# Kernel optimization log

Measured on AMD Instinct MI355X. Metric: run time of the kernel, lower is better.

Reference implementation:

```python
import jax, jax.numpy as jnp
import numpy as np

N_NODES = 50000
N_EDGES = 600000
N_RELS = 500
D = 128


def setup_inputs() -> dict:
    key = jax.random.key(0)
    ks = jax.random.split(key, 8)
    h = jax.random.normal(ks[0], (N_NODES, D), dtype=jnp.float32)
    norm = jax.random.uniform(ks[1], (N_NODES, 1), dtype=jnp.float32)
    rel_emb = jax.random.normal(ks[2], (N_RELS, D), dtype=jnp.float32)
    # xavier-uniform-like scale for square weights
    lim = np.sqrt(6.0 / (D + D)) * np.sqrt(2.0)
    W_neighbor = jax.random.uniform(ks[3], (D, D), dtype=jnp.float32, minval=-lim, maxval=lim)
    loop_weight = jax.random.uniform(ks[4], (D, D), dtype=jnp.float32, minval=-lim, maxval=lim)
    edge_src = jax.random.randint(ks[5], (N_EDGES,), 0, N_NODES, dtype=jnp.int64 if jax.config.jax_enable_x64 else jnp.int32)
    edge_dst = jax.random.randint(ks[6], (N_EDGES,), 0, N_NODES, dtype=edge_src.dtype)
    edge_type = jax.random.randint(ks[7], (N_EDGES,), 0, N_RELS, dtype=edge_src.dtype)
    return {
        "h": h, "norm": norm, "rel_emb": rel_emb,
        "W_neighbor": W_neighbor, "loop_weight": loop_weight,
        "edge_src": edge_src, "edge_dst": edge_dst, "edge_type": edge_type,
    }


def reference(h, norm, rel_emb, W_neighbor, loop_weight, edge_src, edge_dst, edge_type):
    # self-loop message (dense GEMM on node features)
    loop_message = h @ loop_weight  # [N, D]

    # msg_func: gather rel emb + src features, compose ('sub' branch computes node + relation
    # in the original source, reproduced faithfully), dense matmul per edge
    relation = rel_emb[edge_type]          # [E, D] gather
    node = h[edge_src]                     # [E, D] gather
    msg = (node + relation) @ W_neighbor   # [E, D]

    # fn.sum aggregate: scatter-sum messages into destination nodes
    agg = jax.ops.segment_sum(msg, edge_dst, num_segments=h.shape[0])  # [N, D]

    # apply_func: multiply by per-node norm
    node_repr = agg * norm  # [N, D]

    # self_loop add, then activation (relu); dropout=0.0 -> identity
    node_repr = jax.nn.relu(node_repr + loop_message)
    return node_repr
```

## Files before the change

kernel.cpp:

```cpp
#include <hip/hip_runtime.h>

#define NN 50000
#define NE 600000
#define NR 500
#define DD 128
#define CAP 64

#define OFF_CUR  0
#define OFF_BKT  (NN)
#define OFF_HB   (OFF_BKT + NN * CAP)
#define OFF_RELB (OFF_HB + NN * DD / 2)
#define OFF_BP   (OFF_RELB + NR * DD / 2)
#define OFF_AGB  (OFF_BP + 16384)

typedef __bf16 bf16x8 __attribute__((ext_vector_type(8)));
typedef float  f32x4  __attribute__((ext_vector_type(4)));

#define HB_BLOCKS   3125
#define RELB_BLOCKS 32
#define PB_BLOCKS   128

__global__ __launch_bounds__(256) void prep(
    const float* __restrict__ h, const float* __restrict__ rel,
    const float* __restrict__ W, const float* __restrict__ L,
    __bf16* __restrict__ h_bf, __bf16* __restrict__ rel_bf,
    __bf16* __restrict__ Bp)
{
    int b = blockIdx.x;
    if (b < HB_BLOCKS) {
        int t = b * 256 + threadIdx.x;
        const float4* src = (const float4*)h + (size_t)t * 2;
        float4 v0 = src[0], v1 = src[1];
        bf16x8 o;
        o[0]=(__bf16)v0.x; o[1]=(__bf16)v0.y; o[2]=(__bf16)v0.z; o[3]=(__bf16)v0.w;
        o[4]=(__bf16)v1.x; o[5]=(__bf16)v1.y; o[6]=(__bf16)v1.z; o[7]=(__bf16)v1.w;
        *(bf16x8*)(h_bf + (size_t)t * 8) = o;
    } else if (b < HB_BLOCKS + RELB_BLOCKS) {
        int t = (b - HB_BLOCKS) * 256 + threadIdx.x;
        if (t < NR * DD / 8) {
            const float4* src = (const float4*)rel + (size_t)t * 2;
            float4 v0 = src[0], v1 = src[1];
            bf16x8 o;
            o[0]=(__bf16)v0.x; o[1]=(__bf16)v0.y; o[2]=(__bf16)v0.z; o[3]=(__bf16)v0.w;
            o[4]=(__bf16)v1.x; o[5]=(__bf16)v1.y; o[6]=(__bf16)v1.z; o[7]=(__bf16)v1.w;
            *(bf16x8*)(rel_bf + (size_t)t * 8) = o;
        }
    } else {
        int t = (b - HB_BLOCKS - RELB_BLOCKS) * 256 + threadIdx.x;
        int lane  = (t >> 3) & 63;
        int ntile = (t >> 9) & 7;
        int kstep = t >> 12;
        int n = ntile * 16 + (lane & 15);
        int k = kstep * 32 + (lane >> 4) * 8 + (t & 7);
        float v = (k < DD) ? W[k * DD + n] : L[(k - DD) * DD + n];
        Bp[t] = (__bf16)v;
    }
}

__global__ __launch_bounds__(256) void fill_bucket(
    const int* __restrict__ esrc, const int* __restrict__ edst,
    const int* __restrict__ etyp, int* __restrict__ cursor,
    unsigned* __restrict__ bucket)
{
    int e = blockIdx.x * 256 + threadIdx.x;
    if (e < NE) {
        int d = edst[e];
        int pos = atomicAdd(&cursor[d], 1);
        if (pos < CAP)
            bucket[(size_t)d * CAP + pos] = (unsigned)esrc[e] | ((unsigned)etyp[e] << 16);
    }
}

__global__ __launch_bounds__(256) void gather_nodes(
    const __bf16* __restrict__ h_bf, const __bf16* __restrict__ rel_bf,
    const float* __restrict__ norm, const int* __restrict__ cursor,
    const unsigned* __restrict__ bucket, __bf16* __restrict__ agg_bf)
{
    int node = (blockIdx.x * 256 + threadIdx.x) >> 4;
    int lane = threadIdx.x & 15;
    if (node >= NN) return;
    int n = cursor[node];
    n = (n < CAP) ? n : CAP;
    const unsigned* bk = bucket + (size_t)node * CAP;
    float acc[8];
#pragma unroll
    for (int j = 0; j < 8; ++j) acc[j] = 0.f;
    int i = 0;
    for (; i + 1 < n; i += 2) {
        unsigned p0 = bk[i], p1 = bk[i + 1];
        bf16x8 a0 = *(const bf16x8*)(h_bf   + (size_t)(p0 & 0xFFFFu) * DD + lane * 8);
        bf16x8 b0 = *(const bf16x8*)(rel_bf + (size_t)(p0 >> 16)     * DD + lane * 8);
        bf16x8 a1 = *(const bf16x8*)(h_bf   + (size_t)(p1 & 0xFFFFu) * DD + lane * 8);
        bf16x8 b1 = *(const bf16x8*)(rel_bf + (size_t)(p1 >> 16)     * DD + lane * 8);
#pragma unroll
        for (int j = 0; j < 8; ++j)
            acc[j] += ((float)a0[j] + (float)b0[j]) + ((float)a1[j] + (float)b1[j]);
    }
    if (i < n) {
        unsigned p0 = bk[i];
        bf16x8 a0 = *(const bf16x8*)(h_bf   + (size_t)(p0 & 0xFFFFu) * DD + lane * 8);
        bf16x8 b0 = *(const bf16x8*)(rel_bf + (size_t)(p0 >> 16)     * DD + lane * 8);
#pragma unroll
        for (int j = 0; j < 8; ++j) acc[j] += (float)a0[j] + (float)b0[j];
    }
    float sc = norm[node];
    bf16x8 o;
#pragma unroll
    for (int j = 0; j < 8; ++j) o[j] = (__bf16)(acc[j] * sc);
    *(bf16x8*)(agg_bf + (size_t)node * DD + lane * 8) = o;
}

#define AP 264

__global__ __launch_bounds__(256) void fused_mfma(
    const __bf16* __restrict__ h_bf, const __bf16* __restrict__ agg_bf,
    const __bf16* __restrict__ Bp, float* __restrict__ out)
{
    __shared__ __bf16 As[64 * AP];
    int tid = threadIdx.x;
    int row0 = blockIdx.x * 64;

#pragma unroll
    for (int it = 0; it < 8; ++it) {
        int idx = it * 256 + tid;
        int r = idx >> 5;
        int q = idx & 31;
        int gr = row0 + r;
        bf16x8 v = (bf16x8)(__bf16)0.f;
        if (gr < NN) {
            v = (q < 16)
                ? *(const bf16x8*)(agg_bf + (size_t)gr * DD + q * 8)
                : *(const bf16x8*)(h_bf   + (size_t)gr * DD + (q - 16) * 8);
        }
        *(bf16x8*)&As[r * AP + q * 8] = v;
    }
    __syncthreads();

    int lane = tid & 63;
    int wave = tid >> 6;
    int m0 = wave * 16;
    int aoff_base = (m0 + (lane & 15)) * AP + (lane >> 4) * 8;

    f32x4 acc[8];
#pragma unroll
    for (int i = 0; i < 8; ++i) acc[i] = (f32x4)0.f;

#pragma unroll
    for (int kstep = 0; kstep < 8; ++kstep) {
        bf16x8 a = *(const bf16x8*)&As[aoff_base + kstep * 32];
        const __bf16* bbase = Bp + ((size_t)(kstep * 8) * 64 + lane) * 8;
#pragma unroll
        for (int nt = 0; nt < 8; ++nt) {
            bf16x8 b = *(const bf16x8*)(bbase + (size_t)nt * 64 * 8);
            acc[nt] = __builtin_amdgcn_mfma_f32_16x16x32_bf16(a, b, acc[nt], 0, 0, 0);
        }
    }

    int quad = lane >> 4;
    int col_l = lane & 15;
#pragma unroll
    for (int nt = 0; nt < 8; ++nt) {
#pragma unroll
        for (int reg = 0; reg < 4; ++reg) {
            int gr = row0 + m0 + quad * 4 + reg;
            if (gr < NN)
                out[(size_t)gr * DD + nt * 16 + col_l] = fmaxf(acc[nt][reg], 0.f);
        }
    }
}

extern "C" void kernel_launch(void* const* d_in, const int* in_sizes, int n_in,
                              void* d_out, int out_size, void* d_ws, size_t ws_size,
                              hipStream_t stream) {
    const float* h    = (const float*)d_in[0];
    const float* norm = (const float*)d_in[1];
    const float* rel  = (const float*)d_in[2];
    const float* W    = (const float*)d_in[3];
    const float* L    = (const float*)d_in[4];
    const int* esrc   = (const int*)d_in[5];
    const int* edst   = (const int*)d_in[6];
    const int* etyp   = (const int*)d_in[7];
    float* out = (float*)d_out;

    int* ws = (int*)d_ws;
    int* cursor      = ws + OFF_CUR;
    unsigned* bucket = (unsigned*)(ws + OFF_BKT);
    __bf16* h_bf     = (__bf16*)(ws + OFF_HB);
    __bf16* rel_bf   = (__bf16*)(ws + OFF_RELB);
    __bf16* Bp       = (__bf16*)(ws + OFF_BP);
    __bf16* agg_bf   = (__bf16*)(ws + OFF_AGB);

    hipMemsetAsync(cursor, 0, (size_t)NN * sizeof(int), stream);
    prep<<<HB_BLOCKS + RELB_BLOCKS + PB_BLOCKS, 256, 0, stream>>>(
        h, rel, W, L, h_bf, rel_bf, Bp);
    fill_bucket<<<(NE + 255) / 256, 256, 0, stream>>>(esrc, edst, etyp, cursor, bucket);
    gather_nodes<<<NN * 16 / 256, 256, 0, stream>>>(h_bf, rel_bf, norm, cursor,
                                                    bucket, agg_bf);
    fused_mfma<<<(NN + 63) / 64, 256, 0, stream>>>(h_bf, agg_bf, Bp, out);
}
```

Measured before the change: 175.9 us.

## Fuse neighbor gather into MFMA GEMM kernel and fold cursor memset into prep

The per-node gather/aggregate is moved into the GEMM kernel, which writes the normalized aggregate straight into shared memory instead of round-tripping it through a global bf16 buffer. Each node now gets 4 threads with 32 accumulators each, rather than 16 threads with 8. The cursor memset is replaced by extra blocks in the prep kernel, removing a separate launch. The trade-off is less memory-level parallelism per node in the gather, higher register pressure, and only 782 blocks doing the latency-bound gather phase.

New measurement: 207.6 us. 18.0% more time.

```diff
diff --git a/kernel.cpp b/kernel.cpp
--- a/kernel.cpp
+++ b/kernel.cpp
@@ -11,7 +11,6 @@
 #define OFF_HB   (OFF_BKT + NN * CAP)
 #define OFF_RELB (OFF_HB + NN * DD / 2)
 #define OFF_BP   (OFF_RELB + NR * DD / 2)
-#define OFF_AGB  (OFF_BP + 16384)
 
 typedef __bf16 bf16x8 __attribute__((ext_vector_type(8)));
 typedef float  f32x4  __attribute__((ext_vector_type(4)));
@@ -19,12 +18,14 @@
 #define HB_BLOCKS   3125
 #define RELB_BLOCKS 32
 #define PB_BLOCKS   128
+#define CZ_BLOCKS   196
+#define PREP_BLOCKS (HB_BLOCKS + RELB_BLOCKS + PB_BLOCKS + CZ_BLOCKS)
 
 __global__ __launch_bounds__(256) void prep(
     const float* __restrict__ h, const float* __restrict__ rel,
     const float* __restrict__ W, const float* __restrict__ L,
     __bf16* __restrict__ h_bf, __bf16* __restrict__ rel_bf,
-    __bf16* __restrict__ Bp)
+    __bf16* __restrict__ Bp, int* __restrict__ cursor)
 {
     int b = blockIdx.x;
     if (b < HB_BLOCKS) {
@@ -45,7 +46,7 @@
             o[4]=(__bf16)v1.x; o[5]=(__bf16)v1.y; o[6]=(__bf16)v1.z; o[7]=(__bf16)v1.w;
             *(bf16x8*)(rel_bf + (size_t)t * 8) = o;
         }
-    } else {
+    } else if (b < HB_BLOCKS + RELB_BLOCKS + PB_BLOCKS) {
         int t = (b - HB_BLOCKS - RELB_BLOCKS) * 256 + threadIdx.x;
         int lane  = (t >> 3) & 63;
         int ntile = (t >> 9) & 7;
@@ -54,6 +55,9 @@
         int k = kstep * 32 + (lane >> 4) * 8 + (t & 7);
         float v = (k < DD) ? W[k * DD + n] : L[(k - DD) * DD + n];
         Bp[t] = (__bf16)v;
+    } else {
+        int t = (b - HB_BLOCKS - RELB_BLOCKS - PB_BLOCKS) * 256 + threadIdx.x;
+        if (t < NN) cursor[t] = 0;
     }
 }
 
@@ -71,68 +75,86 @@
     }
 }
 
-__global__ __launch_bounds__(256) void gather_nodes(
+#define AP 264
+
+__global__ __launch_bounds__(256) void fused_gather_mfma(
     const __bf16* __restrict__ h_bf, const __bf16* __restrict__ rel_bf,
     const float* __restrict__ norm, const int* __restrict__ cursor,
-    const unsigned* __restrict__ bucket, __bf16* __restrict__ agg_bf)
-{
-    int node = (blockIdx.x * 256 + threadIdx.x) >> 4;
-    int lane = threadIdx.x & 15;
-    if (node >= NN) return;
-    int n = cursor[node];
-    n = (n < CAP) ? n : CAP;
-    const unsigned* bk = bucket + (size_t)node * CAP;
-    float acc[8];
-#pragma unroll
-    for (int j = 0; j < 8; ++j) acc[j] = 0.f;
-    int i = 0;
-    for (; i + 1 < n; i += 2) {
-        unsigned p0 = bk[i], p1 = bk[i + 1];
-        bf16x8 a0 = *(const bf16x8*)(h_bf   + (size_t)(p0 & 0xFFFFu) * DD + lane * 8);
-        bf16x8 b0 = *(const bf16x8*)(rel_bf + (size_t)(p0 >> 16)     * DD + lane * 8);
-        bf16x8 a1 = *(const bf16x8*)(h_bf   + (size_t)(p1 & 0xFFFFu) * DD + lane * 8);
-        bf16x8 b1 = *(const bf16x8*)(rel_bf + (size_t)(p1 >> 16)     * DD + lane * 8);
-#pragma unroll
-        for (int j = 0; j < 8; ++j)
-            acc[j] += ((float)a0[j] + (float)b0[j]) + ((float)a1[j] + (float)b1[j]);
-    }
-    if (i < n) {
-        unsigned p0 = bk[i];
-        bf16x8 a0 = *(const bf16x8*)(h_bf   + (size_t)(p0 & 0xFFFFu) * DD + lane * 8);
-        bf16x8 b0 = *(const bf16x8*)(rel_bf + (size_t)(p0 >> 16)     * DD + lane * 8);
-#pragma unroll
-        for (int j = 0; j < 8; ++j) acc[j] += (float)a0[j] + (float)b0[j];
-    }
-    float sc = norm[node];
-    bf16x8 o;
-#pragma unroll
-    for (int j = 0; j < 8; ++j) o[j] = (__bf16)(acc[j] * sc);
-    *(bf16x8*)(agg_bf + (size_t)node * DD + lane * 8) = o;
-}
-
-#define AP 264
-
-__global__ __launch_bounds__(256) void fused_mfma(
-    const __bf16* __restrict__ h_bf, const __bf16* __restrict__ agg_bf,
-    const __bf16* __restrict__ Bp, float* __restrict__ out)
+    const unsigned* __restrict__ bucket, const __bf16* __restrict__ Bp,
+    float* __restrict__ out)
 {
     __shared__ __bf16 As[64 * AP];
     int tid = threadIdx.x;
     int row0 = blockIdx.x * 64;
 
-#pragma unroll
-    for (int it = 0; it < 8; ++it) {
+    {
+        int g  = tid >> 2;
+        int gl = tid & 3;
+        int node = row0 + g;
+        float acc[32];
+#pragma unroll
+        for (int j = 0; j < 32; ++j) acc[j] = 0.f;
+        if (node < NN) {
+            int n = cursor[node];
+            n = (n < CAP) ? n : CAP;
+            const unsigned* bk = bucket + (size_t)node * CAP;
+            int i = 0;
+            for (; i + 1 < n; i += 2) {
+                unsigned p0 = bk[i], p1 = bk[i + 1];
+                const __bf16* h0 = h_bf   + (size_t)(p0 & 0xFFFFu) * DD + gl * 32;
+                const __bf16* r0 = rel_bf + (size_t)(p0 >> 16)     * DD + gl * 32;
+                const __bf16* h1 = h_bf   + (size_t)(p1 & 0xFFFFu) * DD + gl * 32;
+                const __bf16* r1 = rel_bf + (size_t)(p1 >> 16)     * DD + gl * 32;
+#pragma unroll
+                for (int c = 0; c < 4; ++c) {
+                    bf16x8 a0 = *(const bf16x8*)(h0 + c * 8);
+                    bf16x8 b0 = *(const bf16x8*)(r0 + c * 8);
+                    bf16x8 a1 = *(const bf16x8*)(h1 + c * 8);
+                    bf16x8 b1 = *(const bf16x8*)(r1 + c * 8);
+#pragma unroll
+                    for (int j = 0; j < 8; ++j)
+                        acc[c * 8 + j] += ((float)a0[j] + (float)b0[j]) +
+                                          ((float)a1[j] + (float)b1[j]);
+                }
+            }
+            if (i < n) {
+                unsigned p0 = bk[i];
+                const __bf16* h0 = h_bf   + (size_t)(p0 & 0xFFFFu) * DD + gl * 32;
+                const __bf16* r0 = rel_bf + (size_t)(p0 >> 16)     * DD + gl * 32;
+#pragma unroll
+                for (int c = 0; c < 4; ++c) {
+                    bf16x8 a0 = *(const bf16x8*)(h0 + c * 8);
+                    bf16x8 b0 = *(const bf16x8*)(r0 + c * 8);
+#pragma unroll
+                    for (int j = 0; j < 8; ++j)
+                        acc[c * 8 + j] += (float)a0[j] + (float)b0[j];
+                }
+            }
+            float sc = norm[node];
+#pragma unroll
+            for (int c = 0; c < 4; ++c) {
+                bf16x8 o;
+#pragma unroll
+                for (int j = 0; j < 8; ++j) o[j] = (__bf16)(acc[c * 8 + j] * sc);
+                *(bf16x8*)&As[g * AP + (gl * 4 + c) * 8] = o;
+            }
+        } else {
+            bf16x8 z = (bf16x8)(__bf16)0.f;
+#pragma unroll
+            for (int c = 0; c < 4; ++c)
+                *(bf16x8*)&As[g * AP + (gl * 4 + c) * 8] = z;
+        }
+    }
+
+#pragma unroll
+    for (int it = 0; it < 4; ++it) {
         int idx = it * 256 + tid;
-        int r = idx >> 5;
-        int q = idx & 31;
+        int r = idx >> 4;
+        int q = idx & 15;
         int gr = row0 + r;
         bf16x8 v = (bf16x8)(__bf16)0.f;
-        if (gr < NN) {
-            v = (q < 16)
-                ? *(const bf16x8*)(agg_bf + (size_t)gr * DD + q * 8)
-                : *(const bf16x8*)(h_bf   + (size_t)gr * DD + (q - 16) * 8);
-        }
-        *(bf16x8*)&As[r * AP + q * 8] = v;
+        if (gr < NN) v = *(const bf16x8*)(h_bf + (size_t)gr * DD + q * 8);
+        *(bf16x8*)&As[r * AP + DD + q * 8] = v;
     }
     __syncthreads();
 
@@ -188,13 +210,9 @@
     __bf16* h_bf     = (__bf16*)(ws + OFF_HB);
     __bf16* rel_bf   = (__bf16*)(ws + OFF_RELB);
     __bf16* Bp       = (__bf16*)(ws + OFF_BP);
-    __bf16* agg_bf   = (__bf16*)(ws + OFF_AGB);
-
-    hipMemsetAsync(cursor, 0, (size_t)NN * sizeof(int), stream);
-    prep<<<HB_BLOCKS + RELB_BLOCKS + PB_BLOCKS, 256, 0, stream>>>(
-        h, rel, W, L, h_bf, rel_bf, Bp);
+
+    prep<<<PREP_BLOCKS, 256, 0, stream>>>(h, rel, W, L, h_bf, rel_bf, Bp, cursor);
     fill_bucket<<<(NE + 255) / 256, 256, 0, stream>>>(esrc, edst, etyp, cursor, bucket);
-    gather_nodes<<<NN * 16 / 256, 256, 0, stream>>>(h_bf, rel_bf, norm, cursor,
-                                                    bucket, agg_bf);
-    fused_mfma<<<(NN + 63) / 64, 256, 0, stream>>>(h_bf, agg_bf, Bp, out);
-}
+    fused_gather_mfma<<<(NN + 63) / 64, 256, 0, stream>>>(h_bf, rel_bf, norm, cursor,
+                                                          bucket, Bp, out);
+}
```

## Fuse neighbor gather into MFMA GEMM and fold cursor memset into prep

Applied to the files above, without the earlier changes.

The separate gather kernel and GEMM kernel are merged: each block gathers 16 nodes' neighbor sums into shared memory along with their self features, then its four waves each compute two 16-column MFMA tiles. This removes the bf16 aggregate round trip through global memory and one kernel launch. The cursor memset also becomes extra blocks in the prep kernel, and the gather loop is unrolled by four. In exchange, each block re-reads the whole packed weight matrix for only 16 rows, which raises weight traffic and lowers MFMA reuse per block.

Result: faster. 166.8 us (-5.2%).

```diff
diff --git a/kernel.cpp b/kernel.cpp
--- a/kernel.cpp
+++ b/kernel.cpp
@@ -11,7 +11,6 @@
 #define OFF_HB   (OFF_BKT + NN * CAP)
 #define OFF_RELB (OFF_HB + NN * DD / 2)
 #define OFF_BP   (OFF_RELB + NR * DD / 2)
-#define OFF_AGB  (OFF_BP + 16384)
 
 typedef __bf16 bf16x8 __attribute__((ext_vector_type(8)));
 typedef float  f32x4  __attribute__((ext_vector_type(4)));
@@ -19,12 +18,14 @@
 #define HB_BLOCKS   3125
 #define RELB_BLOCKS 32
 #define PB_BLOCKS   128
+#define CZ_BLOCKS   196
+#define PREP_BLOCKS (HB_BLOCKS + RELB_BLOCKS + PB_BLOCKS + CZ_BLOCKS)
 
 __global__ __launch_bounds__(256) void prep(
     const float* __restrict__ h, const float* __restrict__ rel,
     const float* __restrict__ W, const float* __restrict__ L,
     __bf16* __restrict__ h_bf, __bf16* __restrict__ rel_bf,
-    __bf16* __restrict__ Bp)
+    __bf16* __restrict__ Bp, int* __restrict__ cursor)
 {
     int b = blockIdx.x;
     if (b < HB_BLOCKS) {
@@ -45,7 +46,7 @@
             o[4]=(__bf16)v1.x; o[5]=(__bf16)v1.y; o[6]=(__bf16)v1.z; o[7]=(__bf16)v1.w;
             *(bf16x8*)(rel_bf + (size_t)t * 8) = o;
         }
-    } else {
+    } else if (b < HB_BLOCKS + RELB_BLOCKS + PB_BLOCKS) {
         int t = (b - HB_BLOCKS - RELB_BLOCKS) * 256 + threadIdx.x;
         int lane  = (t >> 3) & 63;
         int ntile = (t >> 9) & 7;
@@ -54,6 +55,9 @@
         int k = kstep * 32 + (lane >> 4) * 8 + (t & 7);
         float v = (k < DD) ? W[k * DD + n] : L[(k - DD) * DD + n];
         Bp[t] = (__bf16)v;
+    } else {
+        int t = (b - HB_BLOCKS - RELB_BLOCKS - PB_BLOCKS) * 256 + threadIdx.x;
+        if (t < NN) cursor[t] = 0;
     }
 }
 
@@ -71,14 +75,21 @@
     }
 }
 
-__global__ __launch_bounds__(256) void gather_nodes(
+#define AP 264
+
+__global__ __launch_bounds__(256) void fused_gather_mfma(
     const __bf16* __restrict__ h_bf, const __bf16* __restrict__ rel_bf,
     const float* __restrict__ norm, const int* __restrict__ cursor,
-    const unsigned* __restrict__ bucket, __bf16* __restrict__ agg_bf)
+    const unsigned* __restrict__ bucket, const __bf16* __restrict__ Bp,
+    float* __restrict__ out)
 {
-    int node = (blockIdx.x * 256 + threadIdx.x) >> 4;
-    int lane = threadIdx.x & 15;
-    if (node >= NN) return;
+    __shared__ __bf16 As[16 * AP];
+    int tid = threadIdx.x;
+    int row0 = blockIdx.x * 16;
+    int g    = tid >> 4;
+    int gl   = tid & 15;
+    int node = row0 + g;
+
     int n = cursor[node];
     n = (n < CAP) ? n : CAP;
     const unsigned* bk = bucket + (size_t)node * CAP;
@@ -86,20 +97,25 @@
 #pragma unroll
     for (int j = 0; j < 8; ++j) acc[j] = 0.f;
     int i = 0;
-    for (; i + 1 < n; i += 2) {
-        unsigned p0 = bk[i], p1 = bk[i + 1];
-        bf16x8 a0 = *(const bf16x8*)(h_bf   + (size_t)(p0 & 0xFFFFu) * DD + lane * 8);
-        bf16x8 b0 = *(const bf16x8*)(rel_bf + (size_t)(p0 >> 16)     * DD + lane * 8);
-        bf16x8 a1 = *(const bf16x8*)(h_bf   + (size_t)(p1 & 0xFFFFu) * DD + lane * 8);
-        bf16x8 b1 = *(const bf16x8*)(rel_bf + (size_t)(p1 >> 16)     * DD + lane * 8);
+    for (; i + 3 < n; i += 4) {
+        unsigned p0 = bk[i], p1 = bk[i+1], p2 = bk[i+2], p3 = bk[i+3];
+        bf16x8 a0 = *(const bf16x8*)(h_bf   + (size_t)(p0 & 0xFFFFu) * DD + gl * 8);
+        bf16x8 b0 = *(const bf16x8*)(rel_bf + (size_t)(p0 >> 16)     * DD + gl * 8);
+        bf16x8 a1 = *(const bf16x8*)(h_bf   + (size_t)(p1 & 0xFFFFu) * DD + gl * 8);
+        bf16x8 b1 = *(const bf16x8*)(rel_bf + (size_t)(p1 >> 16)     * DD + gl * 8);
+        bf16x8 a2 = *(const bf16x8*)(h_bf   + (size_t)(p2 & 0xFFFFu) * DD + gl * 8);
+        bf16x8 b2 = *(const bf16x8*)(rel_bf + (size_t)(p2 >> 16)     * DD + gl * 8);
+        bf16x8 a3 = *(const bf16x8*)(h_bf   + (size_t)(p3 & 0xFFFFu) * DD + gl * 8);
+        bf16x8 b3 = *(const bf16x8*)(rel_bf + (size_t)(p3 >> 16)     * DD + gl * 8);
 #pragma unroll
         for (int j = 0; j < 8; ++j)
-            acc[j] += ((float)a0[j] + (float)b0[j]) + ((float)a1[j] + (float)b1[j]);
+            acc[j] += (((float)a0[j] + (float)b0[j]) + ((float)a1[j] + (float)b1[j]))
+                    + (((float)a2[j] + (float)b2[j]) + ((float)a3[j] + (float)b3[j]));
     }
-    if (i < n) {
+    for (; i < n; ++i) {
         unsigned p0 = bk[i];
-        bf16x8 a0 = *(const bf16x8*)(h_bf   + (size_t)(p0 & 0xFFFFu) * DD + lane * 8);
-        bf16x8 b0 = *(const bf16x8*)(rel_bf + (size_t)(p0 >> 16)     * DD + lane * 8);
+        bf16x8 a0 = *(const bf16x8*)(h_bf   + (size_t)(p0 & 0xFFFFu) * DD + gl * 8);
+        bf16x8 b0 = *(const bf16x8*)(rel_bf + (size_t)(p0 >> 16)     * DD + gl * 8);
 #pragma unroll
         for (int j = 0; j < 8; ++j) acc[j] += (float)a0[j] + (float)b0[j];
     }
@@ -107,65 +123,34 @@
     bf16x8 o;
 #pragma unroll
     for (int j = 0; j < 8; ++j) o[j] = (__bf16)(acc[j] * sc);
-    *(bf16x8*)(agg_bf + (size_t)node * DD + lane * 8) = o;
-}
-
-#define AP 264
-
-__global__ __launch_bounds__(256) void fused_mfma(
-    const __bf16* __restrict__ h_bf, const __bf16* __restrict__ agg_bf,
-    const __bf16* __restrict__ Bp, float* __restrict__ out)
-{
-    __shared__ __bf16 As[64 * AP];
-    int tid = threadIdx.x;
-    int row0 = blockIdx.x * 64;
-
-#pragma unroll
-    for (int it = 0; it < 8; ++it) {
-        int idx = it * 256 + tid;
-        int r = idx >> 5;
-        int q = idx & 31;
-        int gr = row0 + r;
-        bf16x8 v = (bf16x8)(__bf16)0.f;
-        if (gr < NN) {
-            v = (q < 16)
-                ? *(const bf16x8*)(agg_bf + (size_t)gr * DD + q * 8)
-                : *(const bf16x8*)(h_bf   + (size_t)gr * DD + (q - 16) * 8);
-        }
-        *(bf16x8*)&As[r * AP + q * 8] = v;
-    }
+    *(bf16x8*)&As[g * AP + gl * 8] = o;
+    *(bf16x8*)&As[g * AP + DD + gl * 8] =
+        *(const bf16x8*)(h_bf + (size_t)node * DD + gl * 8);
     __syncthreads();
 
     int lane = tid & 63;
     int wave = tid >> 6;
-    int m0 = wave * 16;
-    int aoff_base = (m0 + (lane & 15)) * AP + (lane >> 4) * 8;
+    int aoff = (lane & 15) * AP + (lane >> 4) * 8;
 
-    f32x4 acc[8];
-#pragma unroll
-    for (int i = 0; i < 8; ++i) acc[i] = (f32x4)0.f;
-
+    f32x4 c0 = (f32x4)0.f, c1 = (f32x4)0.f;
+    int nt0 = wave * 2;
 #pragma unroll
     for (int kstep = 0; kstep < 8; ++kstep) {
-        bf16x8 a = *(const bf16x8*)&As[aoff_base + kstep * 32];
-        const __bf16* bbase = Bp + ((size_t)(kstep * 8) * 64 + lane) * 8;
-#pragma unroll
-        for (int nt = 0; nt < 8; ++nt) {
-            bf16x8 b = *(const bf16x8*)(bbase + (size_t)nt * 64 * 8);
-            acc[nt] = __builtin_amdgcn_mfma_f32_16x16x32_bf16(a, b, acc[nt], 0, 0, 0);
-        }
+        bf16x8 a = *(const bf16x8*)&As[aoff + kstep * 32];
+        const __bf16* bbase = Bp + ((size_t)(kstep * 8 + nt0) * 64 + lane) * 8;
+        bf16x8 b0 = *(const bf16x8*)bbase;
+        bf16x8 b1 = *(const bf16x8*)(bbase + 64 * 8);
+        c0 = __builtin_amdgcn_mfma_f32_16x16x32_bf16(a, b0, c0, 0, 0, 0);
+        c1 = __builtin_amdgcn_mfma_f32_16x16x32_bf16(a, b1, c1, 0, 0, 0);
     }
 
     int quad = lane >> 4;
-    int col_l = lane & 15;
+    int col  = lane & 15;
 #pragma unroll
-    for (int nt = 0; nt < 8; ++nt) {
-#pragma unroll
-        for (int reg = 0; reg < 4; ++reg) {
-            int gr = row0 + m0 + quad * 4 + reg;
-            if (gr < NN)
-                out[(size_t)gr * DD + nt * 16 + col_l] = fmaxf(acc[nt][reg], 0.f);
-        }
+    for (int reg = 0; reg < 4; ++reg) {
+        float* op = out + (size_t)(row0 + quad * 4 + reg) * DD + col;
+        op[nt0 * 16]       = fmaxf(c0[reg], 0.f);
+        op[(nt0 + 1) * 16] = fmaxf(c1[reg], 0.f);
     }
 }
 
@@ -188,13 +173,9 @@
     __bf16* h_bf     = (__bf16*)(ws + OFF_HB);
     __bf16* rel_bf   = (__bf16*)(ws + OFF_RELB);
     __bf16* Bp       = (__bf16*)(ws + OFF_BP);
-    __bf16* agg_bf   = (__bf16*)(ws + OFF_AGB);
 
-    hipMemsetAsync(cursor, 0, (size_t)NN * sizeof(int), stream);
-    prep<<<HB_BLOCKS + RELB_BLOCKS + PB_BLOCKS, 256, 0, stream>>>(
-        h, rel, W, L, h_bf, rel_bf, Bp);
+    prep<<<PREP_BLOCKS, 256, 0, stream>>>(h, rel, W, L, h_bf, rel_bf, Bp, cursor);
     fill_bucket<<<(NE + 255) / 256, 256, 0, stream>>>(esrc, edst, etyp, cursor, bucket);
-    gather_nodes<<<NN * 16 / 256, 256, 0, stream>>>(h_bf, rel_bf, norm, cursor,
-                                                    bucket, agg_bf);
-    fused_mfma<<<(NN + 63) / 64, 256, 0, stream>>>(h_bf, agg_bf, Bp, out);
+    fused_gather_mfma<<<NN / 16, 256, 0, stream>>>(h_bf, rel_bf, norm, cursor,
+                                                   bucket, Bp, out);
 }
```
